# Kernel optimization log

Hardware: AMD Instinct MI355X
Metric: run time of the kernel (lower is better)

## Reference

```python
import jax, jax.numpy as jnp
import numpy as np

N_NODES = 50000
N_EDGES = 1600000
N_GRAPHS = 64


def setup_inputs() -> dict:
    key = jax.random.key(0)
    ks = jax.random.split(key, 16)
    x = jax.random.normal(ks[0], (N_NODES, 900), dtype=jnp.float32)
    edge_index = jax.random.randint(ks[1], (2, N_EDGES), 0, N_NODES, dtype=jnp.int64)
    batch = jnp.sort(jax.random.randint(ks[2], (N_NODES,), 0, N_GRAPHS, dtype=jnp.int64))

    def lin(k, out_d, in_d):
        return jax.random.normal(k, (out_d, in_d), dtype=jnp.float32) / np.sqrt(in_d)

    return {
        "x": x, "edge_index": edge_index, "batch": batch,
        # SAGEConv1: lin_l (aggregated, with bias), lin_r (root, no bias)
        "W1l": lin(ks[3], 1024, 900), "b1": jnp.zeros((1024,), jnp.float32), "W1r": lin(ks[4], 1024, 900),
        # SAGEConv2
        "W2l": lin(ks[5], 2048, 1024), "b2": jnp.zeros((2048,), jnp.float32), "W2r": lin(ks[6], 2048, 1024),
        # MLP head
        "Wf1": lin(ks[7], 1024, 2048), "bf1": jnp.zeros((1024,), jnp.float32),
        "Wf2": lin(ks[8], 6, 1024), "bf2": jnp.zeros((6,), jnp.float32),
    }


def _sage_conv(x, src, dst, Wl, b, Wr):
    # mean aggregation of neighbor (source) features onto target nodes
    agg = jax.ops.segment_sum(x[src], dst, num_segments=N_NODES)
    deg = jax.ops.segment_sum(jnp.ones((src.shape[0],), x.dtype), dst, num_segments=N_NODES)
    mean = agg / jnp.maximum(deg, 1.0)[:, None]
    return mean @ Wl.T + b + x @ Wr.T


def reference(x, edge_index, batch, W1l, b1, W1r, W2l, b2, W2r, Wf1, bf1, Wf2, bf2):
    src, dst = edge_index[0], edge_index[1]
    h = jax.nn.relu(_sage_conv(x, src, dst, W1l, b1, W1r))   # [N, 1024]
    h = _sage_conv(h, src, dst, W2l, b2, W2r)                 # [N, 2048]
    pooled = jax.ops.segment_max(h, batch, num_segments=N_GRAPHS)  # [G, 2048]
    pooled = jnp.where(jnp.isfinite(pooled), pooled, 0.0)     # guard empty graphs
    out = jax.nn.relu(pooled @ Wf1.T + bf1) @ Wf2.T + bf2     # [G, 6]
    return out
```

## Files before the change

### kernel.cpp

```cpp
#include <hip/hip_runtime.h>

typedef unsigned short u16x8 __attribute__((ext_vector_type(8)));
typedef char i8x16 __attribute__((ext_vector_type(16)));
typedef int i32x4 __attribute__((ext_vector_type(4)));

constexpr int NN = 50000;
constexpr int NG = 64;
constexpr int MP = 50048;
constexpr int D0 = 900;
constexpr int K0 = 960;
constexpr int D1 = 1024;
constexpr int D2 = 2048;
constexpr int KC1 = 2 * K0;
constexpr int KC2 = 2 * D1;

__device__ __forceinline__ float bf2f(unsigned short u) {
  return __uint_as_float(((unsigned)u) << 16);
}
__device__ __forceinline__ unsigned short f2bf(float f) {
  unsigned x = __float_as_uint(f);
  return (unsigned short)((x + 0x7fffu + ((x >> 16) & 1u)) >> 16);
}

__device__ __forceinline__ void gl_lds16(const void* g, void* l) {
  __builtin_amdgcn_global_load_lds((const __attribute__((address_space(1))) void*)g,
                                   (__attribute__((address_space(3))) void*)l, 16, 0, 0);
}

__global__ __launch_bounds__(256) void cvt_x(const float* __restrict__ in,
                                             char* __restrict__ cat1,
                                             float* __restrict__ xscale) {
  int r = blockIdx.x;
  __shared__ float row[K0];
  __shared__ float smax[256];
  int t = threadIdx.x;
  float m = 0.f;
  for (int c = t; c < K0; c += 256) {
    float v = (r < NN && c < D0) ? in[(size_t)r * D0 + c] : 0.f;
    row[c] = v;
    m = fmaxf(m, fabsf(v));
  }
  smax[t] = m;
  __syncthreads();
  for (int dd = 128; dd; dd >>= 1) {
    if (t < dd) smax[t] = fmaxf(smax[t], smax[t + dd]);
    __syncthreads();
  }
  float mx = smax[0];
  float inv = mx > 0.f ? 127.f / mx : 0.f;
  char* dst = cat1 + (size_t)r * KC1 + K0;
  for (int c = t; c < K0; c += 256) dst[c] = (char)(int)rintf(row[c] * inv);
  if (t == 0) xscale[r] = mx * (1.f / 127.f);
}

__global__ __launch_bounds__(256) void wq_cat(const float* __restrict__ Wl,
                                              const float* __restrict__ Wr, int Cin, int KH,
                                              char* __restrict__ q, float* __restrict__ sc) {
  int r = blockIdx.x, t = threadIdx.x;
  __shared__ float smax[256];
  float m = 0.f;
  for (int c = t; c < Cin; c += 256) {
    m = fmaxf(m, fabsf(Wl[(size_t)r * Cin + c]));
    m = fmaxf(m, fabsf(Wr[(size_t)r * Cin + c]));
  }
  smax[t] = m;
  __syncthreads();
  for (int dd = 128; dd; dd >>= 1) {
    if (t < dd) smax[t] = fmaxf(smax[t], smax[t + dd]);
    __syncthreads();
  }
  float mx = smax[0];
  float inv = mx > 0.f ? 127.f / mx : 0.f;
  char* row = q + (size_t)r * 2 * KH;
  for (int c = t; c < KH; c += 256) {
    row[c]      = (c < Cin) ? (char)(int)rintf(Wl[(size_t)r * Cin + c] * inv) : 0;
    row[KH + c] = (c < Cin) ? (char)(int)rintf(Wr[(size_t)r * Cin + c] * inv) : 0;
  }
  if (t == 0) sc[r] = mx * (1.f / 127.f);
}

__global__ __launch_bounds__(256) void quant_rows(const unsigned short* __restrict__ in,
                                                  char* __restrict__ cat2,
                                                  float* __restrict__ scale) {
  int r = blockIdx.x;
  __shared__ float row[D1];
  __shared__ float smax[256];
  int t = threadIdx.x;
  float m = 0.f;
  for (int c = t; c < D1; c += 256) {
    float v = bf2f(in[(size_t)r * D1 + c]);
    row[c] = v;
    m = fmaxf(m, fabsf(v));
  }
  smax[t] = m;
  __syncthreads();
  for (int dd = 128; dd; dd >>= 1) {
    if (t < dd) smax[t] = fmaxf(smax[t], smax[t + dd]);
    __syncthreads();
  }
  float mx = smax[0];
  float inv = mx > 0.f ? 127.f / mx : 0.f;
  char* dst = cat2 + (size_t)r * KC2 + D1;
  for (int c = t; c < D1; c += 256) dst[c] = (char)(int)rintf(row[c] * inv);
  if (t == 0) scale[r] = mx * (1.f / 127.f);
}

__global__ void zero_i(int* p, int n) {
  int i = blockIdx.x * blockDim.x + threadIdx.x;
  if (i < n) p[i] = 0;
}
__global__ void count_k(const int* __restrict__ dst, int* __restrict__ deg, int E, int n) {
  int e = blockIdx.x * blockDim.x + threadIdx.x;
  if (e < E) {
    int d = dst[e];
    if ((unsigned)d < (unsigned)n) atomicAdd(&deg[d], 1);
  }
}
__global__ void scan1_k(const int* __restrict__ deg, int* __restrict__ off,
                        int* __restrict__ bsum, int n) {
  __shared__ int s[256];
  int t = threadIdx.x;
  int gid = blockIdx.x * 256 + t;
  int v = (gid < n) ? deg[gid] : 0;
  s[t] = v;
  __syncthreads();
  for (int d = 1; d < 256; d <<= 1) {
    int x = (t >= d) ? s[t - d] : 0;
    __syncthreads();
    s[t] += x;
    __syncthreads();
  }
  if (gid < n) off[gid] = s[t] - v;
  if (t == 255) bsum[blockIdx.x] = s[255];
}
__global__ void scan2_k(int* __restrict__ bsum, int nb) {
  __shared__ int s[256];
  int t = threadIdx.x;
  int v = (t < nb) ? bsum[t] : 0;
  s[t] = v;
  __syncthreads();
  for (int d = 1; d < 256; d <<= 1) {
    int x = (t >= d) ? s[t - d] : 0;
    __syncthreads();
    s[t] += x;
    __syncthreads();
  }
  if (t < nb) bsum[t] = s[t] - v;
  if (t == 255) bsum[nb] = s[255];
}
__global__ void scan3_k(int* __restrict__ off, const int* __restrict__ bsum, int n, int nb) {
  int gid = blockIdx.x * 256 + threadIdx.x;
  if (gid < n) off[gid] += bsum[gid >> 8];
  if (gid == 0) off[n] = bsum[nb];
}
__global__ void copy_i(const int* a, int* b, int n) {
  int i = blockIdx.x * blockDim.x + threadIdx.x;
  if (i < n) b[i] = a[i];
}
__global__ void fill_k(const int* __restrict__ src, const int* __restrict__ dst,
                       int* __restrict__ cursor, int* __restrict__ csr, int E, int n) {
  int e = blockIdx.x * blockDim.x + threadIdx.x;
  if (e < E) {
    int d = dst[e];
    if ((unsigned)d < (unsigned)n) {
      int p = atomicAdd(&cursor[d], 1);
      int s = src[e];
      if ((unsigned)s >= (unsigned)n) s = 0;
      csr[p] = s;
    }
  }
}

template <int K, int STRIDE>
__global__ __launch_bounds__(256) void agg_mean_i8w(char* __restrict__ cat,
                                                    const float* __restrict__ rscale,
                                                    const int* __restrict__ off,
                                                    const int* __restrict__ csr) {
  const int node = blockIdx.x * 4 + (threadIdx.x >> 6);
  const int lane = threadIdx.x & 63;
  const int d = lane * 16;
  const bool act = (d < K);
  const int e0 = off[node], e1 = off[node + 1];
  float a[16];
#pragma unroll
  for (int k = 0; k < 16; ++k) a[k] = 0.f;
  if (act) {
    const char* fp = cat + (size_t)K + d;
    int e = e0;
    for (; e + 7 < e1; e += 8) {
      int s0 = csr[e],     s1 = csr[e + 1], s2 = csr[e + 2], s3 = csr[e + 3];
      int s4 = csr[e + 4], s5 = csr[e + 5], s6 = csr[e + 6], s7 = csr[e + 7];
      i8x16 v0 = *(const i8x16*)(fp + (size_t)s0 * STRIDE);
      i8x16 v1 = *(const i8x16*)(fp + (size_t)s1 * STRIDE);
      i8x16 v2 = *(const i8x16*)(fp + (size_t)s2 * STRIDE);
      i8x16 v3 = *(const i8x16*)(fp + (size_t)s3 * STRIDE);
      i8x16 v4 = *(const i8x16*)(fp + (size_t)s4 * STRIDE);
      i8x16 v5 = *(const i8x16*)(fp + (size_t)s5 * STRIDE);
      i8x16 v6 = *(const i8x16*)(fp + (size_t)s6 * STRIDE);
      i8x16 v7 = *(const i8x16*)(fp + (size_t)s7 * STRIDE);
      float c0 = rscale[s0], c1 = rscale[s1], c2 = rscale[s2], c3 = rscale[s3];
      float c4 = rscale[s4], c5 = rscale[s5], c6 = rscale[s6], c7 = rscale[s7];
#pragma unroll
      for (int k = 0; k < 16; ++k) {
        a[k] += c0 * (float)v0[k] + c1 * (float)v1[k] + c2 * (float)v2[k] + c3 * (float)v3[k];
        a[k] += c4 * (float)v4[k] + c5 * (float)v5[k] + c6 * (float)v6[k] + c7 * (float)v7[k];
      }
    }
    for (; e < e1; ++e) {
      int s = csr[e];
      float c = rscale[s];
      i8x16 v = *(const i8x16*)(fp + (size_t)s * STRIDE);
#pragma unroll
      for (int k = 0; k < 16; ++k) a[k] += c * (float)v[k];
    }
  }
  if (act) {
    int deg = e1 - e0;
    float inv = 1.f / (float)(deg > 1 ? deg : 1);
    float sc = rscale[node];
    float qi = sc > 0.f ? 1.f / sc : 0.f;
    i8x16 q;
#pragma unroll
    for (int k = 0; k < 16; ++k) {
      float m = a[k] * inv * qi;
      m = fminf(fmaxf(rintf(m), -127.f), 127.f);
      q[k] = (char)(int)m;
    }
    *(i8x16*)&cat[(size_t)node * STRIDE + d] = q;
  }
}

template <int KP, int N, bool RELU>
__global__ __launch_bounds__(256, 5) void gemm_i8(const char* __restrict__ A,
                                                  const char* __restrict__ W,
                                                  const float* __restrict__ sA_,
                                                  const float* __restrict__ sW_,
                                                  const float* __restrict__ bias,
                                                  unsigned short* __restrict__ C) {
  __shared__ char sA[128 * 64];
  __shared__ char sB[128 * 64];
  __shared__ float sc0[128], sc1[128];
  const int tid = threadIdx.x;
  const int wave = tid >> 6, lane = tid & 63;
  const int quad = lane >> 4, l16 = lane & 15;
  const int wm = (wave >> 1) * 64, wn = (wave & 1) * 64;
  const long long bm = (long long)blockIdx.y * 128;
  const long long bn = (long long)blockIdx.x * 128;

  if (tid < 128) sc0[tid] = sA_[bm + tid];
  else sc1[tid - 128] = sW_[bn + tid - 128];

  const int srow = wave * 16 + (lane >> 2);
  const int skoff = (lane & 3) * 16;
  char* lA = &sA[wave * 1024 + lane * 16];
  char* lB = &sB[wave * 1024 + lane * 16];
  const char* gA = A + (bm + srow) * (long long)KP + skoff;
  const char* gW = W + (bn + srow) * (long long)KP + skoff;

  i32x4 iacc[4][4];
#pragma unroll
  for (int i = 0; i < 4; ++i)
#pragma unroll
    for (int j = 0; j < 4; ++j) iacc[i][j] = (i32x4){0, 0, 0, 0};

#pragma unroll 1
  for (int k0 = 0; k0 < KP; k0 += 64) {
    __syncthreads();
    gl_lds16(gA + k0, lA);
    gl_lds16(gA + k0 + (size_t)64 * KP, lA + 4096);
    gl_lds16(gW + k0, lB);
    gl_lds16(gW + k0 + (size_t)64 * KP, lB + 4096);
    __syncthreads();
    i32x4 af[4], bg[4];
#pragma unroll
    for (int i = 0; i < 4; ++i)
      af[i] = *(const i32x4*)&sA[(wm + 16 * i + l16) * 64 + quad * 16];
#pragma unroll
    for (int j = 0; j < 4; ++j)
      bg[j] = *(const i32x4*)&sB[(wn + 16 * j + l16) * 64 + quad * 16];
#pragma unroll
    for (int i = 0; i < 4; ++i)
#pragma unroll
      for (int j = 0; j < 4; ++j)
        iacc[i][j] = __builtin_amdgcn_mfma_i32_16x16x64_i8(af[i], bg[j], iacc[i][j], 0, 0, 0);
  }

#pragma unroll
  for (int j = 0; j < 4; ++j) {
    const int coll = wn + 16 * j + l16;
    const long long col = bn + coll;
    const float bv = bias[col];
    const float cw = sc1[coll];
#pragma unroll
    for (int i = 0; i < 4; ++i) {
      const int rowb = wm + 16 * i + quad * 4;
      const long long row0 = bm + rowb;
#pragma unroll
      for (int r = 0; r < 4; ++r) {
        float v = (float)iacc[i][j][r] * sc0[rowb + r] * cw + bv;
        if (RELU) v = fmaxf(v, 0.f);
        C[(row0 + r) * (long long)N + col] = f2bf(v);
      }
    }
  }
}

__global__ void bounds_k(const int* __restrict__ batch, int* __restrict__ gstart, int n, int G) {
  int g = blockIdx.x * blockDim.x + threadIdx.x;
  if (g > G) return;
  int lo = 0, hi = n;
  while (lo < hi) {
    int mid = (lo + hi) >> 1;
    if (batch[mid] < g) lo = mid + 1; else hi = mid;
  }
  gstart[g] = lo;
}

__global__ void segmax_k(const unsigned short* __restrict__ h2b, const int* __restrict__ gstart,
                         float* __restrict__ pooled) {
  int g = blockIdx.x;
  int c = blockIdx.y * 256 + threadIdx.x;
  int i0 = gstart[g], i1 = gstart[g + 1];
  float m = -3.4e38f;
  for (int i = i0; i < i1; ++i) m = fmaxf(m, bf2f(h2b[(size_t)i * D2 + c]));
  if (i0 >= i1) m = 0.f;
  pooled[(size_t)g * D2 + c] = m;
}

__global__ void head1_k(const float* __restrict__ pooled, const float* __restrict__ Wf1,
                        const float* __restrict__ bf1, float* __restrict__ hid) {
  int g = blockIdx.x, chunk = blockIdx.y;
  __shared__ float sp[2048];
  for (int i = threadIdx.x; i < 2048; i += 256) sp[i] = pooled[(size_t)g * 2048 + i];
  __syncthreads();
  int wave = threadIdx.x >> 6, lane = threadIdx.x & 63;
  for (int oi = wave; oi < 64; oi += 4) {
    int o = chunk * 64 + oi;
    const float4* wr = (const float4*)&Wf1[(size_t)o * 2048];
    float s = 0.f;
    for (int c = lane; c < 512; c += 64) {
      float4 wv = wr[c];
      float4 pv = *(const float4*)&sp[c * 4];
      s += wv.x * pv.x + wv.y * pv.y + wv.z * pv.z + wv.w * pv.w;
    }
    for (int off = 32; off; off >>= 1) s += __shfl_down(s, off);
    if (lane == 0) hid[(size_t)g * 1024 + o] = fmaxf(s + bf1[o], 0.f);
  }
}
__global__ void head2_k(const float* __restrict__ hid, const float* __restrict__ Wf2,
                        const float* __restrict__ bf2, float* __restrict__ out) {
  int g = blockIdx.x, t = threadIdx.x;
  __shared__ float sh[1024];
  __shared__ float red[256];
  for (int i = t; i < 1024; i += 256) sh[i] = hid[(size_t)g * 1024 + i];
  __syncthreads();
  for (int o = 0; o < 6; ++o) {
    float s = 0.f;
    for (int k = t; k < 1024; k += 256) s += sh[k] * Wf2[o * 1024 + k];
    red[t] = s;
    __syncthreads();
    for (int d = 128; d; d >>= 1) {
      if (t < d) red[t] += red[t + d];
      __syncthreads();
    }
    if (t == 0) out[g * 6 + o] = red[0] + bf2[o];
    __syncthreads();
  }
}

extern "C" void kernel_launch(void* const* d_in, const int* in_sizes, int n_in,
                              void* d_out, int out_size, void* d_ws, size_t ws_size,
                              hipStream_t stream) {
  const float* x    = (const float*)d_in[0];
  const int* ei     = (const int*)d_in[1];
  const int* batch  = (const int*)d_in[2];
  const float* W1l  = (const float*)d_in[3];
  const float* b1   = (const float*)d_in[4];
  const float* W1r  = (const float*)d_in[5];
  const float* W2l  = (const float*)d_in[6];
  const float* b2   = (const float*)d_in[7];
  const float* W2r  = (const float*)d_in[8];
  const float* Wf1  = (const float*)d_in[9];
  const float* bf1  = (const float*)d_in[10];
  const float* Wf2  = (const float*)d_in[11];
  const float* bf2  = (const float*)d_in[12];
  float* out = (float*)d_out;

  const int E = in_sizes[1] / 2;
  const int* srcp = ei;
  const int* dstp = ei + E;
  const int NB = (MP + 255) / 256;

  char* w = (char*)d_ws;
  auto take = [&](size_t b) {
    void* p = (void*)w;
    w += (b + 255) & ~(size_t)255;
    return p;
  };
  char* cat1      = (char*)take((size_t)MP * KC1);
  char* cat2      = (char*)take((size_t)MP * KC2);
  unsigned short* h1b = (unsigned short*)take((size_t)MP * D1 * 2);
  unsigned short* h2b = (unsigned short*)take((size_t)MP * D2 * 2);
  char* wcat1     = (char*)take((size_t)D1 * KC1);
  char* wcat2     = (char*)take((size_t)D2 * KC2);
  float* xscale   = (float*)take((size_t)MP * 4);
  float* h1scale  = (float*)take((size_t)MP * 4);
  float* swc1     = (float*)take((size_t)D1 * 4);
  float* swc2     = (float*)take((size_t)D2 * 4);
  int* deg    = (int*)take((size_t)MP * 4);
  int* off    = (int*)take((size_t)(MP + 1) * 4);
  int* bsum   = (int*)take((size_t)(NB + 1) * 4);
  int* cursor = (int*)take((size_t)MP * 4);
  int* csr    = (int*)take((size_t)E * 4);
  int* gstart = (int*)take((size_t)(NG + 1) * 4);
  float* pooled = (float*)take((size_t)NG * D2 * 4);
  float* hid    = (float*)take((size_t)NG * 1024 * 4);

  cvt_x<<<MP, 256, 0, stream>>>(x, cat1, xscale);
  wq_cat<<<D1, 256, 0, stream>>>(W1l, W1r, D0, K0, wcat1, swc1);
  wq_cat<<<D2, 256, 0, stream>>>(W2l, W2r, D1, D1, wcat2, swc2);

  zero_i<<<(MP + 255) / 256, 256, 0, stream>>>(deg, MP);
  count_k<<<(E + 255) / 256, 256, 0, stream>>>(dstp, deg, E, NN);
  scan1_k<<<NB, 256, 0, stream>>>(deg, off, bsum, MP);
  scan2_k<<<1, 256, 0, stream>>>(bsum, NB);
  scan3_k<<<NB, 256, 0, stream>>>(off, bsum, MP, NB);
  copy_i<<<(MP + 255) / 256, 256, 0, stream>>>(off, cursor, MP);
  fill_k<<<(E + 255) / 256, 256, 0, stream>>>(srcp, dstp, cursor, csr, E, NN);

  agg_mean_i8w<K0, KC1><<<MP / 4, 256, 0, stream>>>(cat1, xscale, off, csr);
  gemm_i8<KC1, D1, true><<<dim3(D1 / 128, MP / 128), 256, 0, stream>>>(
      cat1, wcat1, xscale, swc1, b1, h1b);

  quant_rows<<<MP, 256, 0, stream>>>(h1b, cat2, h1scale);
  agg_mean_i8w<D1, KC2><<<MP / 4, 256, 0, stream>>>(cat2, h1scale, off, csr);
  gemm_i8<KC2, D2, false><<<dim3(D2 / 128, MP / 128), 256, 0, stream>>>(
      cat2, wcat2, h1scale, swc2, b2, h2b);

  bounds_k<<<1, 128, 0, stream>>>(batch, gstart, NN, NG);
  segmax_k<<<dim3(NG, D2 / 256), 256, 0, stream>>>(h2b, gstart, pooled);
  head1_k<<<dim3(NG, 16), 256, 0, stream>>>(pooled, Wf1, bf1, hid);
  head2_k<<<NG, 256, 0, stream>>>(hid, Wf2, bf2, out);
}
```

Baseline: 1.832 ms.

## Stage int8 GEMM epilogue through LDS for coalesced stores and remap workgroups

The int8 GEMM epilogue now writes bf16 results into a padded LDS tile in two 64-row halves. It then stores them to global memory as 16-byte coalesced vectors, replacing scattered 2-byte stores. Workgroup IDs are also remapped in groups of eight, likely to spread tiles across the XCDs for better L2 locality. The cost is extra LDS traffic and barriers in the epilogue, plus reuse of the operand shared memory for the staging tile.

Result: faster. 1.688 ms (-7.9%).

```diff
diff --git a/kernel.cpp b/kernel.cpp
--- a/kernel.cpp
+++ b/kernel.cpp
@@ -237,15 +237,26 @@
                                                   const float* __restrict__ sW_,
                                                   const float* __restrict__ bias,
                                                   unsigned short* __restrict__ C) {
-  __shared__ char sA[128 * 64];
-  __shared__ char sB[128 * 64];
-  __shared__ float sc0[128], sc1[128];
+  __shared__ __align__(16) char smem[17408];
+  char* sA = smem;
+  char* sB = smem + 8192;
+  float* sc0 = (float*)(smem + 16384);
+  float* sc1 = sc0 + 128;
+
+  const int gx = gridDim.x;
+  const int nwg = gx * gridDim.y;
+  const int flat = blockIdx.y * gx + blockIdx.x;
+  int newid = flat;
+  if ((nwg & 7) == 0) newid = (flat & 7) * (nwg >> 3) + (flat >> 3);
+  const int bxi = newid % gx;
+  const int byi = newid / gx;
+
   const int tid = threadIdx.x;
   const int wave = tid >> 6, lane = tid & 63;
   const int quad = lane >> 4, l16 = lane & 15;
   const int wm = (wave >> 1) * 64, wn = (wave & 1) * 64;
-  const long long bm = (long long)blockIdx.y * 128;
-  const long long bn = (long long)blockIdx.x * 128;
+  const long long bm = (long long)byi * 128;
+  const long long bn = (long long)bxi * 128;
 
   if (tid < 128) sc0[tid] = sA_[bm + tid];
   else sc1[tid - 128] = sW_[bn + tid - 128];
@@ -285,22 +296,41 @@
         iacc[i][j] = __builtin_amdgcn_mfma_i32_16x16x64_i8(af[i], bg[j], iacc[i][j], 0, 0, 0);
   }
 
+  float rs[4][4], cs[4], bvj[4];
+#pragma unroll
+  for (int i = 0; i < 4; ++i)
+#pragma unroll
+    for (int r = 0; r < 4; ++r) rs[i][r] = sc0[wm + 16 * i + quad * 4 + r];
 #pragma unroll
   for (int j = 0; j < 4; ++j) {
     const int coll = wn + 16 * j + l16;
-    const long long col = bn + coll;
-    const float bv = bias[col];
-    const float cw = sc1[coll];
-#pragma unroll
-    for (int i = 0; i < 4; ++i) {
-      const int rowb = wm + 16 * i + quad * 4;
-      const long long row0 = bm + rowb;
-#pragma unroll
-      for (int r = 0; r < 4; ++r) {
-        float v = (float)iacc[i][j][r] * sc0[rowb + r] * cw + bv;
-        if (RELU) v = fmaxf(v, 0.f);
-        C[(row0 + r) * (long long)N + col] = f2bf(v);
-      }
+    cs[j] = sc1[coll];
+    bvj[j] = bias[bn + coll];
+  }
+  unsigned short* ct = (unsigned short*)smem;
+  const int trow = tid >> 4;
+  const int tcol = (tid & 15) * 8;
+#pragma unroll
+  for (int p = 0; p < 2; ++p) {
+    __syncthreads();
+    if ((wm >> 6) == p) {
+#pragma unroll
+      for (int i = 0; i < 4; ++i)
+#pragma unroll
+        for (int j = 0; j < 4; ++j)
+#pragma unroll
+          for (int r = 0; r < 4; ++r) {
+            float v = (float)iacc[i][j][r] * rs[i][r] * cs[j] + bvj[j];
+            if (RELU) v = fmaxf(v, 0.f);
+            ct[(16 * i + quad * 4 + r) * 136 + wn + 16 * j + l16] = f2bf(v);
+          }
+    }
+    __syncthreads();
+#pragma unroll
+    for (int s = 0; s < 4; ++s) {
+      const int rl = s * 16 + trow;
+      i32x4 vv = *(const i32x4*)&ct[rl * 136 + tcol];
+      *(i32x4*)&C[(bm + p * 64 + rl) * (long long)N + bn + tcol] = vv;
     }
   }
 }
```
